# Performance work log

Measured on AMD Instinct MI355X. Metric: run time of the kernel, lower is better.

Reference implementation:

```python
import jax, jax.numpy as jnp
import numpy as np

B, D, H, O, E = 4096, 1024, 4096, 1024, 8
TOP_K = 2


def setup_inputs() -> dict:
    key = jax.random.key(0)
    ks = jax.random.split(key, 7)
    s = 0.02
    return {
        "expert_input": jax.random.normal(ks[0], (B, D), dtype=jnp.float32),
        "Wg": jax.random.normal(ks[1], (D, E), dtype=jnp.float32) * s,
        "bg": jnp.zeros((E,), dtype=jnp.float32),
        "W1": jax.random.normal(ks[2], (E, D, H), dtype=jnp.float32) * s,
        "b1": jnp.zeros((E, H), dtype=jnp.float32),
        "W2": jax.random.normal(ks[3], (E, H, O), dtype=jnp.float32) * s,
        "b2": jnp.zeros((E, O), dtype=jnp.float32),
    }


def reference(expert_input, Wg, bg, W1, b1, W2, b2):
    x = expert_input                                  # [B, D]
    gate_logits = x @ Wg + bg                         # [B, E]
    topk_logits, topk_idx = jax.lax.top_k(gate_logits, TOP_K)
    topk_w = jax.nn.softmax(topk_logits, axis=1)      # softmax over the k selected logits
    rows = jnp.arange(x.shape[0])[:, None]
    dense_w = jnp.zeros_like(gate_logits).at[rows, topk_idx].set(topk_w)  # [B, E]
    # Dense (all-experts) evaluation; zero gate weight == unrouted, so math
    # matches the masked per-expert loop in the torch module exactly.
    h = jax.nn.relu(jnp.einsum('bd,edh->ebh', x, W1) + b1[:, None, :])    # [E, B, H]
    expert_out = jnp.einsum('ebh,eho->ebo', h, W2) + b2[:, None, :]       # [E, B, O]
    routed = jnp.einsum('be,ebo->bo', dense_w, expert_out)                # [B, O]
    return routed
```

## Files before the change

### kernel.cpp

```cpp
#include <hip/hip_runtime.h>
#include <cstdint>

#define DEVI __device__ __forceinline__

typedef __bf16 bf16x8_t __attribute__((ext_vector_type(8)));
typedef float f32x4_t __attribute__((ext_vector_type(4)));

typedef const __attribute__((address_space(1))) unsigned int* gas_t;
typedef __attribute__((address_space(3))) unsigned int* las_t;

DEVI void glds16(const void* g, void* l) {
  __builtin_amdgcn_global_load_lds((gas_t)g, (las_t)l, 16, 0, 0);
}

DEVI uint16_t f2b(float f) {
  uint32_t u = __builtin_bit_cast(uint32_t, f);
  u += 0x7fffu + ((u >> 16) & 1u);
  return (uint16_t)(u >> 16);
}

static constexpr int MAXT = 72;

__global__ __launch_bounds__(256) void moe_gate(const float* __restrict__ x,
    const float* __restrict__ Wg, const float* __restrict__ bg,
    int* __restrict__ gidx, float* __restrict__ gw) {
  const int lane = threadIdx.x & 63;
  const int b = blockIdx.x * 4 + (threadIdx.x >> 6);
  float acc[8];
#pragma unroll
  for (int e = 0; e < 8; ++e) acc[e] = 0.f;
  const float* xr = x + (size_t)b * 1024;
#pragma unroll
  for (int it = 0; it < 4; ++it) {
    const int d0 = it * 256 + lane * 4;
    float4 xv = *(const float4*)(xr + d0);
    float xs[4] = {xv.x, xv.y, xv.z, xv.w};
#pragma unroll
    for (int q = 0; q < 4; ++q) {
      const float4* wrow = (const float4*)(Wg + (size_t)(d0 + q) * 8);
      float4 wa = wrow[0], wb = wrow[1];
      acc[0] += xs[q] * wa.x; acc[1] += xs[q] * wa.y;
      acc[2] += xs[q] * wa.z; acc[3] += xs[q] * wa.w;
      acc[4] += xs[q] * wb.x; acc[5] += xs[q] * wb.y;
      acc[6] += xs[q] * wb.z; acc[7] += xs[q] * wb.w;
    }
  }
#pragma unroll
  for (int off = 32; off; off >>= 1)
#pragma unroll
    for (int e = 0; e < 8; ++e) acc[e] += __shfl_xor(acc[e], off, 64);
  if (lane == 0) {
    float l[8];
#pragma unroll
    for (int e = 0; e < 8; ++e) l[e] = acc[e] + bg[e];
    int i0 = 0;
#pragma unroll
    for (int e = 1; e < 8; ++e) if (l[e] > l[i0]) i0 = e;
    int i1 = (i0 == 0) ? 1 : 0;
#pragma unroll
    for (int e = 0; e < 8; ++e) if (e != i0 && l[e] > l[i1]) i1 = e;
    float ex = expf(l[i1] - l[i0]);
    float s = 1.f + ex;
    gidx[2 * b] = i0; gidx[2 * b + 1] = i1;
    gw[2 * b] = 1.f / s; gw[2 * b + 1] = ex / s;
  }
}

__global__ __launch_bounds__(256) void moe_scan(const int* __restrict__ gidx,
                                                int* __restrict__ meta) {
  __shared__ int cnt[8];
  if (threadIdx.x < 8) cnt[threadIdx.x] = 0;
  __syncthreads();
  int loc[8] = {0, 0, 0, 0, 0, 0, 0, 0};
  for (int i = threadIdx.x; i < 8192; i += 256) {
    int e = gidx[i];
#pragma unroll
    for (int q = 0; q < 8; ++q) loc[q] += (e == q) ? 1 : 0;
  }
#pragma unroll
  for (int q = 0; q < 8; ++q) atomicAdd(&cnt[q], loc[q]);
  __syncthreads();
  if (threadIdx.x == 0) {
    int off = 0, t = 0;
    for (int e = 0; e < 8; ++e) {
      int c = cnt[e];
      meta[e] = c;
      meta[8 + e] = off;
      meta[17 + e] = 0;
      int nt = (c + 127) >> 7;
      for (int mt = 0; mt < nt; ++mt) {
        meta[32 + t] = e;
        meta[104 + t] = off + mt * 128;
        meta[176 + t] = off + c;
        ++t;
      }
      off += c;
    }
    meta[16] = off;
    meta[25] = t;
  }
}

__global__ __launch_bounds__(256) void moe_scatter(const int* __restrict__ gidx,
    const float* __restrict__ gw, int* __restrict__ meta,
    int* __restrict__ row_index, float* __restrict__ row_w) {
  int i = blockIdx.x * 256 + threadIdx.x;
  int e = gidx[i];
  int pos = meta[8 + e] + atomicAdd(&meta[17 + e], 1);
  row_index[pos] = i >> 1;
  row_w[pos] = gw[i];
}

__global__ __launch_bounds__(256) void moe_cvtx(const float* __restrict__ x,
                                                uint16_t* __restrict__ xb) {
  size_t i = ((size_t)blockIdx.x * 256 + threadIdx.x) * 4;
  float4 v = *(const float4*)(x + i);
  uint64_t pk = (uint64_t)f2b(v.x) | ((uint64_t)f2b(v.y) << 16) |
                ((uint64_t)f2b(v.z) << 32) | ((uint64_t)f2b(v.w) << 48);
  *(uint64_t*)(xb + i) = pk;
}

__global__ __launch_bounds__(256) void moe_transpose(const float* __restrict__ in,
                                                     uint16_t* __restrict__ outp,
                                                     int K, int N) {
  __shared__ uint16_t t[64][72];
  const int e = blockIdx.z;
  const int k0 = blockIdx.y * 64, n0 = blockIdx.x * 64;
  const int r = threadIdx.x >> 2;
  const int c0 = (threadIdx.x & 3) * 16;
  const float* src = in + ((size_t)e * K + k0 + r) * N + n0 + c0;
#pragma unroll
  for (int q = 0; q < 4; ++q) {
    float4 v = *(const float4*)(src + q * 4);
    uint64_t pk = (uint64_t)f2b(v.x) | ((uint64_t)f2b(v.y) << 16) |
                  ((uint64_t)f2b(v.z) << 32) | ((uint64_t)f2b(v.w) << 48);
    *(uint64_t*)&t[r][c0 + q * 4] = pk;
  }
  __syncthreads();
  alignas(16) uint16_t buf[16];
#pragma unroll
  for (int j = 0; j < 16; ++j) buf[j] = t[c0 + j][r];
  uint16_t* dst = outp + ((size_t)e * N + n0 + r) * K + k0 + c0;
  *(uint4*)dst = *(const uint4*)&buf[0];
  *(uint4*)(dst + 8) = *(const uint4*)&buf[8];
}

template <int KD, int ND, int MODE>
__global__ __launch_bounds__(256, 2) void moe_gemm(
    const uint16_t* __restrict__ Am, const uint16_t* __restrict__ Bt,
    const float* __restrict__ bias, const int* __restrict__ meta,
    const int* __restrict__ row_index, const float* __restrict__ row_w,
    uint16_t* __restrict__ hout, float* __restrict__ out) {
  const int nT = meta[25];
  if ((int)blockIdx.y >= nT) return;
  const int e = meta[32 + blockIdx.y];
  const int pos0 = meta[104 + blockIdx.y];
  const int vend = meta[176 + blockIdx.y];
  const int nb = blockIdx.x;

  __shared__ uint16_t As[2][128 * 32];
  __shared__ uint16_t Bs[2][128 * 32];

  const int tid = threadIdx.x;
  const int lane = tid & 63;
  const int w = tid >> 6;
  const int wr = w >> 1, wc = w & 1;

  size_t aoff[2], boff[2];
#pragma unroll
  for (int j = 0; j < 2; ++j) {
    int c = j * 256 + tid;
    int row = c >> 2;
    int skc = (c & 3) ^ (row & 3);
    int pos = pos0 + row;
    if (pos > 8191) pos = 8191;
    int ar = (MODE == 1) ? row_index[pos] : pos;
    aoff[j] = ((size_t)ar * KD + (size_t)skc * 8) * 2;
    boff[j] = (((size_t)e * ND + (size_t)nb * 128 + row) * KD + (size_t)skc * 8) * 2;
  }
  const char* Ag = (const char*)Am;
  const char* Bg = (const char*)Bt;

  f32x4_t acc[4][4];
  f32x4_t z;
  z[0] = 0.f; z[1] = 0.f; z[2] = 0.f; z[3] = 0.f;
#pragma unroll
  for (int m = 0; m < 4; ++m)
#pragma unroll
    for (int n = 0; n < 4; ++n) acc[m][n] = z;

  auto stage = [&](int buf, int t) {
#pragma unroll
    for (int j = 0; j < 2; ++j) {
      glds16(Ag + aoff[j] + (size_t)t * 64, &As[buf][(j * 256 + w * 64) * 8]);
      glds16(Bg + boff[j] + (size_t)t * 64, &Bs[buf][(j * 256 + w * 64) * 8]);
    }
  };

  stage(0, 0);
  __syncthreads();
  int cur = 0;
  const int NIT = KD / 32;
  for (int t = 0; t < NIT; ++t) {
    if (t + 1 < NIT) stage(cur ^ 1, t + 1);
    const uint16_t* Ap = As[cur];
    const uint16_t* Bp = Bs[cur];
    bf16x8_t af[4], bfr[4];
#pragma unroll
    for (int m = 0; m < 4; ++m) {
      int row = wr * 64 + m * 16 + (lane & 15);
      int skc = ((lane >> 4) ^ row) & 3;
      af[m] = *(const bf16x8_t*)(Ap + row * 32 + skc * 8);
    }
#pragma unroll
    for (int n = 0; n < 4; ++n) {
      int row = wc * 64 + n * 16 + (lane & 15);
      int skc = ((lane >> 4) ^ row) & 3;
      bfr[n] = *(const bf16x8_t*)(Bp + row * 32 + skc * 8);
    }
#pragma unroll
    for (int m = 0; m < 4; ++m)
#pragma unroll
      for (int n = 0; n < 4; ++n)
        acc[m][n] = __builtin_amdgcn_mfma_f32_16x16x32_bf16(af[m], bfr[n], acc[m][n], 0, 0, 0);
    __syncthreads();
    cur ^= 1;
  }

  const int cb = nb * 128 + wc * 64;
  if constexpr (MODE == 1) {
#pragma unroll
    for (int m = 0; m < 4; ++m) {
      int pr = pos0 + wr * 64 + m * 16 + ((lane >> 4) << 2);
#pragma unroll
      for (int i = 0; i < 4; ++i) {
        int pos = pr + i;
        if (pos < vend) {
#pragma unroll
          for (int n = 0; n < 4; ++n) {
            int col = cb + n * 16 + (lane & 15);
            float v = acc[m][n][i] + bias[e * ND + col];
            v = fmaxf(v, 0.f);
            hout[(size_t)pos * ND + col] = f2b(v);
          }
        }
      }
    }
  } else {
#pragma unroll
    for (int m = 0; m < 4; ++m) {
      int pr = pos0 + wr * 64 + m * 16 + ((lane >> 4) << 2);
#pragma unroll
      for (int i = 0; i < 4; ++i) {
        int pos = pr + i;
        if (pos < vend) {
          int bi = row_index[pos];
          float wgt = row_w[pos];
          float* orow = out + (size_t)bi * ND;
#pragma unroll
          for (int n = 0; n < 4; ++n) {
            int col = cb + n * 16 + (lane & 15);
            float v = (acc[m][n][i] + bias[e * ND + col]) * wgt;
            atomicAdd(orow + col, v);
          }
        }
      }
    }
  }
}

extern "C" void kernel_launch(void* const* d_in, const int* in_sizes, int n_in,
                              void* d_out, int out_size, void* d_ws, size_t ws_size,
                              hipStream_t stream) {
  const float* x  = (const float*)d_in[0];
  const float* Wg = (const float*)d_in[1];
  const float* bg = (const float*)d_in[2];
  const float* W1 = (const float*)d_in[3];
  const float* b1 = (const float*)d_in[4];
  const float* W2 = (const float*)d_in[5];
  const float* b2 = (const float*)d_in[6];
  float* out = (float*)d_out;

  char* ws = (char*)d_ws;
  uint16_t* w1t = (uint16_t*)ws; ws += (size_t)8 * 4096 * 1024 * 2;
  uint16_t* w2t = (uint16_t*)ws; ws += (size_t)8 * 1024 * 4096 * 2;
  uint16_t* xb  = (uint16_t*)ws; ws += (size_t)4096 * 1024 * 2;
  uint16_t* h   = (uint16_t*)ws; ws += (size_t)8192 * 4096 * 2;
  int*   gidx = (int*)ws;   ws += 8192 * 4;
  float* gw   = (float*)ws; ws += 8192 * 4;
  int*   rix  = (int*)ws;   ws += 8192 * 4;
  float* rw   = (float*)ws; ws += 8192 * 4;
  int*   meta = (int*)ws;   ws += 4096;

  hipMemsetAsync(d_out, 0, (size_t)4096 * 1024 * 4, stream);
  moe_cvtx<<<4096, 256, 0, stream>>>(x, xb);
  moe_transpose<<<dim3(4096 / 64, 1024 / 64, 8), 256, 0, stream>>>(W1, w1t, 1024, 4096);
  moe_transpose<<<dim3(1024 / 64, 4096 / 64, 8), 256, 0, stream>>>(W2, w2t, 4096, 1024);
  moe_gate<<<1024, 256, 0, stream>>>(x, Wg, bg, gidx, gw);
  moe_scan<<<1, 256, 0, stream>>>(gidx, meta);
  moe_scatter<<<32, 256, 0, stream>>>(gidx, gw, meta, rix, rw);
  moe_gemm<1024, 4096, 1><<<dim3(32, MAXT), 256, 0, stream>>>(xb, w1t, b1, meta, rix, rw, h, nullptr);
  moe_gemm<4096, 1024, 2><<<dim3(8, MAXT), 256, 0, stream>>>(h, w2t, b2, meta, rix, rw, nullptr, out);
}
```

Baseline: 446.5 us.

## Replace grouped GEMMs with 256x256 tiled, 8-wave pipelined kernel with split-K

Grouped expert GEMMs now use 256x256 output tiles with 512 threads, 128KB dynamic LDS and a deeper multi-stage global-to-LDS prefetch schedule with explicit waitcnt/barrier and setprio around MFMA. Workgroups are remapped across XCDs. The second GEMM uses split-K of 2, with bias added only by the first slice. Routing metadata is re-tiled to 256-row tiles. The aim is more data reuse per tile and better overlap of loads with MFMA, at the cost of more padding waste on partial expert tiles and double the atomics in the second GEMM.

```diff
diff --git a/kernel.cpp b/kernel.cpp
--- a/kernel.cpp
+++ b/kernel.cpp
@@ -19,7 +19,7 @@
   return (uint16_t)(u >> 16);
 }
 
-static constexpr int MAXT = 72;
+static constexpr int MAXT = 40;
 
 __global__ __launch_bounds__(256) void moe_gate(const float* __restrict__ x,
     const float* __restrict__ Wg, const float* __restrict__ bg,
@@ -87,17 +87,17 @@
       meta[e] = c;
       meta[8 + e] = off;
       meta[17 + e] = 0;
-      int nt = (c + 127) >> 7;
+      int nt = (c + 255) >> 8;
       for (int mt = 0; mt < nt; ++mt) {
         meta[32 + t] = e;
-        meta[104 + t] = off + mt * 128;
-        meta[176 + t] = off + c;
+        meta[80 + t] = off + mt * 256;
+        meta[128 + t] = off + c;
         ++t;
       }
       off += c;
     }
     meta[16] = off;
-    meta[25] = t;
+    meta[26] = t;
   }
 }
 
@@ -145,123 +145,154 @@
   *(uint4*)(dst + 8) = *(const uint4*)&buf[8];
 }
 
-template <int KD, int ND, int MODE>
-__global__ __launch_bounds__(256, 2) void moe_gemm(
+template <int KD, int ND, int MODE, int KSL>
+__global__ __launch_bounds__(512, 2) void moe_gemm8(
     const uint16_t* __restrict__ Am, const uint16_t* __restrict__ Bt,
     const float* __restrict__ bias, const int* __restrict__ meta,
     const int* __restrict__ row_index, const float* __restrict__ row_w,
     uint16_t* __restrict__ hout, float* __restrict__ out) {
-  const int nT = meta[25];
-  if ((int)blockIdx.y >= nT) return;
-  const int e = meta[32 + blockIdx.y];
-  const int pos0 = meta[104 + blockIdx.y];
-  const int vend = meta[176 + blockIdx.y];
-  const int nb = blockIdx.x;
-
-  __shared__ uint16_t As[2][128 * 32];
-  __shared__ uint16_t Bs[2][128 * 32];
+  constexpr int NB = ND / 256;
+  constexpr int KSLEN = KD / KSL;
+  constexpr int NKT = KSLEN / 64;
+  constexpr int NIT = NKT / 2;
+  extern __shared__ uint16_t lds[];
+
+  const int nwg = gridDim.x;
+  const int orig = blockIdx.x;
+  const int q = nwg >> 3, r8 = nwg & 7, xcd = orig & 7, loc = orig >> 3;
+  int wg = (xcd < r8 ? xcd * (q + 1) : r8 * (q + 1) + (xcd - r8) * q) + loc;
+  const int nb = wg % NB; wg /= NB;
+  const int ks2 = wg % KSL; wg /= KSL;
+  const int ty = wg;
+  if (ty >= meta[26]) return;
+  const int e = meta[32 + ty];
+  const int pos0 = meta[80 + ty];
+  const int vend = meta[128 + ty];
+  const int k0 = ks2 * KSLEN;
 
   const int tid = threadIdx.x;
   const int lane = tid & 63;
   const int w = tid >> 6;
-  const int wr = w >> 1, wc = w & 1;
-
-  size_t aoff[2], boff[2];
-#pragma unroll
-  for (int j = 0; j < 2; ++j) {
-    int c = j * 256 + tid;
-    int row = c >> 2;
-    int skc = (c & 3) ^ (row & 3);
-    int pos = pos0 + row;
-    if (pos > 8191) pos = 8191;
-    int ar = (MODE == 1) ? row_index[pos] : pos;
-    aoff[j] = ((size_t)ar * KD + (size_t)skc * 8) * 2;
-    boff[j] = (((size_t)e * ND + (size_t)nb * 128 + row) * KD + (size_t)skc * 8) * 2;
+  const int wr = w >> 2, wc = w & 3;
+
+  const int crow = tid >> 2;
+  const int swz = (tid & 3) ^ (crow & 3);
+  uint32_t aoff[2], boff[2];
+#pragma unroll
+  for (int l = 0; l < 2; ++l) {
+    int r = l * 128 + crow;
+    int pos = pos0 + r; if (pos > 8191) pos = 8191;
+    int arow = (MODE == 1) ? row_index[pos] : pos;
+    aoff[l] = (uint32_t)arow * (KD * 2) + (uint32_t)(k0 * 2) + swz * 16;
+    boff[l] = (uint32_t)(e * ND + nb * 256 + r) * (KD * 2) + (uint32_t)(k0 * 2) + swz * 16;
   }
   const char* Ag = (const char*)Am;
   const char* Bg = (const char*)Bt;
 
-  f32x4_t acc[4][4];
-  f32x4_t z;
-  z[0] = 0.f; z[1] = 0.f; z[2] = 0.f; z[3] = 0.f;
-#pragma unroll
-  for (int m = 0; m < 4; ++m)
+  const int dst0 = (w * 64) * 8;
+  const int dst1 = (512 + w * 64) * 8;
+
+  auto stageUnit = [&](int H) {
+    int kt = H >> 2; if (kt > NKT - 1) kt = NKT - 1;
+    const int u = H & 3;
+    const int ab = u & 1, ks = u >> 1;
+    uint16_t* dst = lds + ((((kt & 1) * 2 + ab) * 2 + ks) << 13);
+    uint32_t kadd = (uint32_t)kt * 128 + (uint32_t)ks * 64;
+    if (ab == 0) {
+      glds16(Ag + (aoff[0] + kadd), dst + dst0);
+      glds16(Ag + (aoff[1] + kadd), dst + dst1);
+    } else {
+      glds16(Bg + (boff[0] + kadd), dst + dst0);
+      glds16(Bg + (boff[1] + kadd), dst + dst1);
+    }
+  };
+
+  const int fRow = (lane & 15) * 32;
+  const int fSwz = ((lane >> 4) ^ (lane & 3)) * 8;
+  const int aBaseR = (wr * 128) * 32;
+  const int bBaseR = (wc * 64) * 32;
+
+  f32x4_t acc[8][4];
+  f32x4_t z; z[0] = 0.f; z[1] = 0.f; z[2] = 0.f; z[3] = 0.f;
+#pragma unroll
+  for (int m = 0; m < 8; ++m)
 #pragma unroll
     for (int n = 0; n < 4; ++n) acc[m][n] = z;
 
-  auto stage = [&](int buf, int t) {
-#pragma unroll
-    for (int j = 0; j < 2; ++j) {
-      glds16(Ag + aoff[j] + (size_t)t * 64, &As[buf][(j * 256 + w * 64) * 8]);
-      glds16(Bg + boff[j] + (size_t)t * 64, &Bs[buf][(j * 256 + w * 64) * 8]);
-    }
-  };
-
-  stage(0, 0);
-  __syncthreads();
-  int cur = 0;
-  const int NIT = KD / 32;
-  for (int t = 0; t < NIT; ++t) {
-    if (t + 1 < NIT) stage(cur ^ 1, t + 1);
-    const uint16_t* Ap = As[cur];
-    const uint16_t* Bp = Bs[cur];
-    bf16x8_t af[4], bfr[4];
-#pragma unroll
-    for (int m = 0; m < 4; ++m) {
-      int row = wr * 64 + m * 16 + (lane & 15);
-      int skc = ((lane >> 4) ^ row) & 3;
-      af[m] = *(const bf16x8_t*)(Ap + row * 32 + skc * 8);
-    }
-#pragma unroll
-    for (int n = 0; n < 4; ++n) {
-      int row = wc * 64 + n * 16 + (lane & 15);
-      int skc = ((lane >> 4) ^ row) & 3;
-      bfr[n] = *(const bf16x8_t*)(Bp + row * 32 + skc * 8);
-    }
-#pragma unroll
-    for (int m = 0; m < 4; ++m)
-#pragma unroll
-      for (int n = 0; n < 4; ++n)
-        acc[m][n] = __builtin_amdgcn_mfma_f32_16x16x32_bf16(af[m], bfr[n], acc[m][n], 0, 0, 0);
-    __syncthreads();
-    cur ^= 1;
-  }
-
-  const int cb = nb * 128 + wc * 64;
+#pragma unroll
+  for (int H = 0; H < 6; ++H) stageUnit(H);
+  asm volatile("s_waitcnt vmcnt(4)" ::: "memory");
+  __builtin_amdgcn_s_barrier();
+  asm volatile("" ::: "memory");
+
+  for (int i = 0; i < NIT; ++i) {
+    bf16x8_t bfr[4];
+#pragma unroll
+    for (int p = 0; p < 8; ++p) {
+      const int g = p >> 2, sub = p & 3, ksp = sub >> 1, mh = sub & 1;
+      const uint16_t* Ar = lds + (((g * 2 + 0) * 2 + ksp) << 13);
+      const uint16_t* Br = lds + (((g * 2 + 1) * 2 + ksp) << 13);
+      bf16x8_t af[4];
+#pragma unroll
+      for (int m = 0; m < 4; ++m)
+        af[m] = *(const bf16x8_t*)(Ar + aBaseR + (mh * 64 + m * 16) * 32 + fRow + fSwz);
+      if (mh == 0) {
+#pragma unroll
+        for (int n = 0; n < 4; ++n)
+          bfr[n] = *(const bf16x8_t*)(Br + bBaseR + n * 16 * 32 + fRow + fSwz);
+      }
+      stageUnit(8 * i + 6 + p);
+      asm volatile("" ::: "memory");
+      __builtin_amdgcn_s_barrier();
+      asm volatile("s_waitcnt lgkmcnt(0)" ::: "memory");
+      __builtin_amdgcn_s_setprio(1);
+#pragma unroll
+      for (int m = 0; m < 4; ++m)
+#pragma unroll
+        for (int n = 0; n < 4; ++n)
+          acc[mh * 4 + m][n] = __builtin_amdgcn_mfma_f32_16x16x32_bf16(
+              af[m], bfr[n], acc[mh * 4 + m][n], 0, 0, 0);
+      __builtin_amdgcn_s_setprio(0);
+      if (sub == 3) asm volatile("s_waitcnt vmcnt(4)" ::: "memory");
+      __builtin_amdgcn_s_barrier();
+      asm volatile("" ::: "memory");
+    }
+  }
+
+  const int cbase = nb * 256 + wc * 64;
   if constexpr (MODE == 1) {
 #pragma unroll
-    for (int m = 0; m < 4; ++m) {
-      int pr = pos0 + wr * 64 + m * 16 + ((lane >> 4) << 2);
-#pragma unroll
-      for (int i = 0; i < 4; ++i) {
-        int pos = pr + i;
+    for (int M = 0; M < 8; ++M) {
+      int pr = pos0 + wr * 128 + M * 16 + ((lane >> 4) << 2);
+#pragma unroll
+      for (int i2 = 0; i2 < 4; ++i2) {
+        int pos = pr + i2;
         if (pos < vend) {
 #pragma unroll
           for (int n = 0; n < 4; ++n) {
-            int col = cb + n * 16 + (lane & 15);
-            float v = acc[m][n][i] + bias[e * ND + col];
-            v = fmaxf(v, 0.f);
-            hout[(size_t)pos * ND + col] = f2b(v);
+            int col = cbase + n * 16 + (lane & 15);
+            float v = acc[M][n][i2] + bias[e * ND + col];
+            hout[(size_t)pos * ND + col] = f2b(fmaxf(v, 0.f));
           }
         }
       }
     }
   } else {
 #pragma unroll
-    for (int m = 0; m < 4; ++m) {
-      int pr = pos0 + wr * 64 + m * 16 + ((lane >> 4) << 2);
-#pragma unroll
-      for (int i = 0; i < 4; ++i) {
-        int pos = pr + i;
+    for (int M = 0; M < 8; ++M) {
+      int pr = pos0 + wr * 128 + M * 16 + ((lane >> 4) << 2);
+#pragma unroll
+      for (int i2 = 0; i2 < 4; ++i2) {
+        int pos = pr + i2;
         if (pos < vend) {
           int bi = row_index[pos];
           float wgt = row_w[pos];
           float* orow = out + (size_t)bi * ND;
 #pragma unroll
           for (int n = 0; n < 4; ++n) {
-            int col = cb + n * 16 + (lane & 15);
-            float v = (acc[m][n][i] + bias[e * ND + col]) * wgt;
-            atomicAdd(orow + col, v);
+            int col = cbase + n * 16 + (lane & 15);
+            float bterm = (ks2 == 0) ? bias[e * ND + col] : 0.f;
+            atomicAdd(orow + col, (acc[M][n][i2] + bterm) * wgt);
           }
         }
       }
@@ -292,6 +323,15 @@
   float* rw   = (float*)ws; ws += 8192 * 4;
   int*   meta = (int*)ws;   ws += 4096;
 
+  static bool attr_done = false;
+  if (!attr_done) {
+    hipFuncSetAttribute((const void*)moe_gemm8<1024, 4096, 1, 1>,
+                        hipFuncAttributeMaxDynamicSharedMemorySize, 131072);
+    hipFuncSetAttribute((const void*)moe_gemm8<4096, 1024, 2, 2>,
+                        hipFuncAttributeMaxDynamicSharedMemorySize, 131072);
+    attr_done = true;
+  }
+
   hipMemsetAsync(d_out, 0, (size_t)4096 * 1024 * 4, stream);
   moe_cvtx<<<4096, 256, 0, stream>>>(x, xb);
   moe_transpose<<<dim3(4096 / 64, 1024 / 64, 8), 256, 0, stream>>>(W1, w1t, 1024, 4096);
@@ -299,6 +339,8 @@
   moe_gate<<<1024, 256, 0, stream>>>(x, Wg, bg, gidx, gw);
   moe_scan<<<1, 256, 0, stream>>>(gidx, meta);
   moe_scatter<<<32, 256, 0, stream>>>(gidx, gw, meta, rix, rw);
-  moe_gemm<1024, 4096, 1><<<dim3(32, MAXT), 256, 0, stream>>>(xb, w1t, b1, meta, rix, rw, h, nullptr);
-  moe_gemm<4096, 1024, 2><<<dim3(8, MAXT), 256, 0, stream>>>(h, w2t, b2, meta, rix, rw, nullptr, out);
-}
+  moe_gemm8<1024, 4096, 1, 1><<<dim3(16 * MAXT), 512, 131072, stream>>>(
+      xb, w1t, b1, meta, rix, rw, h, nullptr);
+  moe_gemm8<4096, 1024, 2, 2><<<dim3(4 * 2 * MAXT), 512, 131072, stream>>>(
+      h, w2t, b2, meta, rix, rw, nullptr, out);
+}
```

After: 510.1 us. +14.2%, slower.
